# Kernel optimization log

Measured on AMD Instinct MI355X. Metric: run time of the kernel, lower is better.

The kernel has to match this reference:

```python
import jax, jax.numpy as jnp
import numpy as np

N_IN, N_HID, N_OUT = 2048, 4096, 1024
N_TOT = N_IN + N_HID + N_OUT
BATCH = 4096


def _structure_mask():
    # input -> {hidden, output}; hidden -> {hidden, output}; nothing feeds inputs,
    # outputs feed nothing.
    m = np.zeros((N_TOT, N_TOT), dtype=np.float32)
    m[0:N_IN, N_IN:N_TOT] = 1.0
    m[N_IN:N_IN + N_HID, N_IN:N_TOT] = 1.0
    return jnp.asarray(m)


def setup_inputs() -> dict:
    key = jax.random.key(0)
    kx, kw = jax.random.split(key)
    x = jax.random.normal(kx, (BATCH, N_IN), dtype=jnp.float32)
    weights = jax.random.normal(kw, (N_TOT, N_TOT), dtype=jnp.float32) * 0.1
    structure_mask = _structure_mask()
    return {"x": x, "weights": weights, "structure_mask": structure_mask}


def reference(x, weights, structure_mask):
    # Faithful to the torch forward: the per-neuron hidden loop reads the
    # activation vector BEFORE any hidden value is written, so every hidden
    # unit sees only [x, 0, 0]; outputs then see [x, hidden, 0].
    Wm = weights * structure_mask  # (N_TOT, N_TOT)
    B = x.shape[0]
    a0 = jnp.concatenate(
        [x, jnp.zeros((B, N_HID + N_OUT), dtype=x.dtype)], axis=1)  # (B, N_TOT)
    hidden = jax.nn.relu(a0 @ Wm[:, N_IN:N_IN + N_HID])             # (B, N_HID)
    a1 = jnp.concatenate(
        [x, hidden, jnp.zeros((B, N_OUT), dtype=x.dtype)], axis=1)  # (B, N_TOT)
    out = a1 @ Wm[:, N_IN + N_HID:]                                 # (B, N_OUT)
    return out
```

## Files before the change

kernel.cpp:

```cpp
#include <hip/hip_runtime.h>
#include <hip/hip_bf16.h>

#define N_IN  2048
#define N_HID 4096
#define N_OUT 1024
#define N_TOT 7168
#define BATCH 4096
#define LDA2  (N_IN + N_HID)
#define OUT_ELEMS ((size_t)BATCH * N_OUT)
#define BUF 16384

typedef __attribute__((ext_vector_type(8))) short short8;
typedef __attribute__((ext_vector_type(4))) float f32x4;

static __device__ __forceinline__ unsigned short f2bf(float f) {
  __hip_bfloat16 h = __float2bfloat16(f);
  return __builtin_bit_cast(unsigned short, h);
}

__global__ void conv_x_kernel(const float* __restrict__ x,
                              unsigned short* __restrict__ A2) {
  int idx = blockIdx.x * 256 + threadIdx.x;
  int row = idx >> 9;
  int col = (idx & 511) << 2;
  const float4 v = *(const float4*)(x + (size_t)row * N_IN + col);
  ushort4 o;
  o.x = f2bf(v.x); o.y = f2bf(v.y); o.z = f2bf(v.z); o.w = f2bf(v.w);
  *(ushort4*)(A2 + (size_t)row * LDA2 + col) = o;
}

__global__ void conv_t_kernel(const float* __restrict__ src, int lds_,
                              unsigned short* __restrict__ dst, int ldd) {
  __shared__ float tile[32][33];
  const int t = threadIdx.x;
  const int k0 = blockIdx.y << 5, n0 = blockIdx.x << 5;
  const int r = t >> 3, c = (t & 7) << 2;
  const float4 v = *(const float4*)(src + (size_t)(k0 + r) * lds_ + n0 + c);
  tile[r][c] = v.x; tile[r][c + 1] = v.y; tile[r][c + 2] = v.z; tile[r][c + 3] = v.w;
  __syncthreads();
  ushort4 o;
  o.x = f2bf(tile[c][r]);
  o.y = f2bf(tile[c + 1][r]);
  o.z = f2bf(tile[c + 2][r]);
  o.w = f2bf(tile[c + 3][r]);
  *(ushort4*)(dst + (size_t)(n0 + r) * ldd + k0 + c) = o;
}

__global__ void add5_kernel(const float* __restrict__ P, float* __restrict__ out) {
  size_t i = ((size_t)blockIdx.x * 256 + threadIdx.x) * 4;
  float4 a = *(const float4*)(P + i);
  float4 b = *(const float4*)(P + OUT_ELEMS + i);
  float4 c = *(const float4*)(P + 2 * OUT_ELEMS + i);
  float4 d = *(const float4*)(P + 3 * OUT_ELEMS + i);
  float4 e = *(const float4*)(P + 4 * OUT_ELEMS + i);
  float4 o;
  o.x = ((a.x + b.x) + (c.x + d.x)) + e.x;
  o.y = ((a.y + b.y) + (c.y + d.y)) + e.y;
  o.z = ((a.z + b.z) + (c.z + d.z)) + e.z;
  o.w = ((a.w + b.w) + (c.w + d.w)) + e.w;
  *(float4*)(out + i) = o;
}

struct KCtx {
  int wave, wm, wn, lm, quad, xr, srow, arow, brow;
};

static __device__ __forceinline__ void kctx_init(KCtx& c, int tid) {
  c.wave = tid >> 6;
  c.wm   = c.wave >> 2;
  c.wn   = c.wave & 3;
  c.lm   = tid & 15;
  c.quad = (tid & 63) >> 4;
  c.xr   = c.lm & 7;
  c.srow = c.wave * 16;
  c.arow = (c.wm * 128 + c.lm) * 64;
  c.brow = (c.wn * 64  + c.lm) * 64;
}

#define GLDS(GP, LP) __builtin_amdgcn_global_load_lds( \
    (const __attribute__((address_space(1))) void*)(GP), \
    (__attribute__((address_space(3))) void*)(LP), 16, 0, 0)

#define STG(GBASE, LD, LBASE, H, KC) do {                                     \
    GLDS((GBASE) + (size_t)((H)*128 + c.srow    ) * (LD) + (KC),              \
         (LBASE) + ((H)*128 + c.srow    ) * 64);                              \
    GLDS((GBASE) + (size_t)((H)*128 + c.srow + 8) * (LD) + (KC),              \
         (LBASE) + ((H)*128 + c.srow + 8) * 64);                              \
  } while (0)

#define LDB(BB) do {                                                          \
    _Pragma("unroll") for (int nt = 0; nt < 4; ++nt)                          \
    _Pragma("unroll") for (int kk = 0; kk < 2; ++kk)                          \
      bv[nt][kk] = *(const short8*)((BB) + c.brow + nt * 1024 +               \
                                    (((kk * 4 + c.quad) ^ c.xr) << 3));       \
  } while (0)

#define LDA_(AB, Q) do {                                                      \
    _Pragma("unroll") for (int j = 0; j < 2; ++j)                             \
    _Pragma("unroll") for (int kk = 0; kk < 2; ++kk)                          \
      av[j][kk] = *(const short8*)((AB) + c.arow + (2 * (Q) + j) * 1024 +     \
                                   (((kk * 4 + c.quad) ^ c.xr) << 3));        \
  } while (0)

#define MM(Q) do {                                                            \
    _Pragma("unroll") for (int kk = 0; kk < 2; ++kk)                          \
    _Pragma("unroll") for (int j = 0; j < 2; ++j)                             \
    _Pragma("unroll") for (int nt = 0; nt < 4; ++nt)                          \
      acc[2 * (Q) + j][nt] = __builtin_amdgcn_mfma_f32_16x16x32_bf16(         \
          av[j][kk], bv[nt][kk], acc[2 * (Q) + j][nt], 0, 0, 0);              \
  } while (0)

#define BAR       __builtin_amdgcn_s_barrier()
#define WAITLGKM  asm volatile("s_waitcnt lgkmcnt(0)" ::: "memory")
#define WAITVM4   asm volatile("s_waitcnt vmcnt(4)" ::: "memory")
#define WAITVM0   asm volatile("s_waitcnt vmcnt(0)" ::: "memory")
#define PRIO1     __builtin_amdgcn_s_setprio(1)
#define PRIO0     __builtin_amdgcn_s_setprio(0)

static __device__ __forceinline__ void kloop_256(
    const unsigned short* __restrict__ Agl,
    const unsigned short* __restrict__ Bgl,
    const int lda, const int ldb, const int kiters,
    unsigned short* __restrict__ S, const KCtx& c, f32x4 acc[8][4]) {
  unsigned short* const A0 = S;
  unsigned short* const A1 = S + BUF;
  unsigned short* const B0 = S + 2 * BUF;
  unsigned short* const B1 = S + 3 * BUF;

  short8 bv[4][2], av[2][2];

  STG(Agl, lda, A0, 0, 0); STG(Agl, lda, A0, 1, 0);
  STG(Bgl, ldb, B0, 0, 0); STG(Bgl, ldb, B0, 1, 0);
  STG(Bgl, ldb, B1, 0, 64); STG(Bgl, ldb, B1, 1, 64);
  WAITVM4;
  BAR;

#pragma unroll 1
  for (int i = 0; i < kiters - 1; ++i) {
    const int k1 = i * 128 + 64, k2 = i * 128 + 128, k3 = i * 128 + 192;
    LDB(B0); LDA_(A0, 0); STG(Agl, lda, A1, 0, k1);
    BAR; WAITLGKM; PRIO1; MM(0); PRIO0; BAR;
    LDA_(A0, 1); STG(Agl, lda, A1, 1, k1);
    BAR; WAITLGKM; PRIO1; MM(1); PRIO0; BAR;
    LDA_(A0, 2); STG(Bgl, ldb, B0, 0, k2);
    BAR; WAITLGKM; PRIO1; MM(2); PRIO0; BAR;
    LDA_(A0, 3); STG(Bgl, ldb, B0, 1, k2);
    WAITVM4; BAR; WAITLGKM; PRIO1; MM(3); PRIO0; BAR;
    LDB(B1); LDA_(A1, 0); STG(Agl, lda, A0, 0, k2);
    BAR; WAITLGKM; PRIO1; MM(0); PRIO0; BAR;
    LDA_(A1, 1); STG(Agl, lda, A0, 1, k2);
    BAR; WAITLGKM; PRIO1; MM(1); PRIO0; BAR;
    LDA_(A1, 2); STG(Bgl, ldb, B1, 0, k3);
    BAR; WAITLGKM; PRIO1; MM(2); PRIO0; BAR;
    LDA_(A1, 3); STG(Bgl, ldb, B1, 1, k3);
    WAITVM4; BAR; WAITLGKM; PRIO1; MM(3); PRIO0; BAR;
  }
  {
    const int k1 = (kiters - 1) * 128 + 64;
    LDB(B0); LDA_(A0, 0); STG(Agl, lda, A1, 0, k1);
    BAR; WAITLGKM; PRIO1; MM(0); PRIO0; BAR;
    LDA_(A0, 1); STG(Agl, lda, A1, 1, k1);
    BAR; WAITLGKM; PRIO1; MM(1); PRIO0; BAR;
    LDA_(A0, 2);
    BAR; WAITLGKM; PRIO1; MM(2); PRIO0; BAR;
    LDA_(A0, 3);
    WAITVM0; BAR; WAITLGKM; PRIO1; MM(3); PRIO0; BAR;
    LDB(B1); LDA_(A1, 0);
    BAR; WAITLGKM; PRIO1; MM(0); PRIO0; BAR;
    LDA_(A1, 1);
    BAR; WAITLGKM; PRIO1; MM(1); PRIO0; BAR;
    LDA_(A1, 2);
    BAR; WAITLGKM; PRIO1; MM(2); PRIO0; BAR;
    LDA_(A1, 3);
    BAR; WAITLGKM; PRIO1; MM(3); PRIO0; BAR;
  }
}

template <bool TO_BF16_RELU>
static __device__ __forceinline__ void epi_store(
    unsigned short* __restrict__ S, const KCtx& c, int tid, f32x4 acc[8][4],
    void* __restrict__ Cout, int ldc, int rowb, int colb) {
  float* Cf = (float*)S;
#pragma unroll 1
  for (int p = 0; p < 4; ++p) {
    if (c.wm == (p >> 1)) {
      const int mtb = (p & 1) * 4;
#pragma unroll
      for (int mt = 0; mt < 4; ++mt)
#pragma unroll
        for (int nt = 0; nt < 4; ++nt)
#pragma unroll
          for (int r = 0; r < 4; ++r)
            Cf[(mt * 16 + c.quad * 4 + r) * 260 + c.wn * 64 + nt * 16 + c.lm] =
                acc[mtb + mt][nt][r];
    }
    __syncthreads();
    const int c4 = (tid & 63) * 4;
    const int r0 = tid >> 6;
#pragma unroll
    for (int j = 0; j < 8; ++j) {
      const int row = r0 + 8 * j;
      float4 v = *(const float4*)(Cf + row * 260 + c4);
      if (TO_BF16_RELU) {
        ushort4 o;
        o.x = f2bf(v.x > 0.f ? v.x : 0.f);
        o.y = f2bf(v.y > 0.f ? v.y : 0.f);
        o.z = f2bf(v.z > 0.f ? v.z : 0.f);
        o.w = f2bf(v.w > 0.f ? v.w : 0.f);
        *(ushort4*)((unsigned short*)Cout +
                    (size_t)(rowb + p * 64 + row) * ldc + colb + c4) = o;
      } else {
        *(float4*)((float*)Cout +
                   (size_t)(rowb + p * 64 + row) * ldc + colb + c4) = v;
      }
    }
    __syncthreads();
  }
}

__global__ __launch_bounds__(512, 2)
void gemm_fused2(const unsigned short* __restrict__ A,
                 const unsigned short* __restrict__ Bt,
                 unsigned short* __restrict__ Hout,
                 float* __restrict__ P0) {
  __shared__ __align__(16) unsigned short S[4 * BUF];
  const int tid = threadIdx.x;
  const int lane = tid & 63;
  KCtx c; kctx_init(c, tid);
  const int bm = blockIdx.y, bn = blockIdx.x;
  const int gcol = ((lane & 7) ^ (lane >> 3)) << 3;

  const unsigned short* Agl = A  + (size_t)(bm * 256 + (lane >> 3)) * LDA2 + gcol;
  const unsigned short* Bgl = Bt + (size_t)(bn * 256 + (lane >> 3)) * N_IN + gcol;

  f32x4 acc[8][4];
#pragma unroll
  for (int i = 0; i < 8; ++i)
#pragma unroll
    for (int j = 0; j < 4; ++j)
      acc[i][j] = (f32x4){0.f, 0.f, 0.f, 0.f};

  kloop_256(Agl, Bgl, LDA2, N_IN, N_IN / 128, S, c, acc);
  __syncthreads();

  if (bn < 16)
    epi_store<true >(S, c, tid, acc, Hout, LDA2, bm * 256, bn * 256);
  else
    epi_store<false>(S, c, tid, acc, P0, N_OUT, bm * 256, (bn - 16) * 256);
}

__global__ __launch_bounds__(512, 2)
void gemm_p2(const unsigned short* __restrict__ A,
             const unsigned short* __restrict__ Bt,
             float* __restrict__ P) {
  __shared__ __align__(16) unsigned short S[4 * BUF];
  const int tid = threadIdx.x;
  const int lane = tid & 63;
  KCtx c; kctx_init(c, tid);
  const int bm = blockIdx.y, bn = blockIdx.x;
  const int ko0 = blockIdx.z * 1024;
  const int gcol = ((lane & 7) ^ (lane >> 3)) << 3;

  const unsigned short* Agl = A  + (size_t)(bm * 256 + (lane >> 3)) * LDA2 + gcol + ko0;
  const unsigned short* Bgl = Bt + (size_t)(bn * 256 + (lane >> 3)) * N_HID + gcol + ko0;

  f32x4 acc[8][4];
#pragma unroll
  for (int i = 0; i < 8; ++i)
#pragma unroll
    for (int j = 0; j < 4; ++j)
      acc[i][j] = (f32x4){0.f, 0.f, 0.f, 0.f};

  kloop_256(Agl, Bgl, LDA2, N_HID, 1024 / 128, S, c, acc);
  __syncthreads();

  epi_store<false>(S, c, tid, acc, P + (size_t)blockIdx.z * OUT_ELEMS, N_OUT,
                   bm * 256, bn * 256);
}

extern "C" void kernel_launch(void* const* d_in, const int* in_sizes, int n_in,
                              void* d_out, int out_size, void* d_ws, size_t ws_size,
                              hipStream_t stream) {
  const float* x = (const float*)d_in[0];
  const float* W = (const float*)d_in[1];

  char* ws = (char*)d_ws;
  const size_t A2_BYTES   = (size_t)BATCH * LDA2 * 2;
  const size_t BT12_BYTES = (size_t)(N_HID + N_OUT) * N_IN * 2;
  const size_t BT3_BYTES  = (size_t)N_OUT * N_HID * 2;
  unsigned short* A2   = (unsigned short*)ws;
  unsigned short* Bt12 = (unsigned short*)(ws + A2_BYTES);
  unsigned short* Bt3  = (unsigned short*)(ws + A2_BYTES + BT12_BYTES);
  float*          P    = (float*)(ws + A2_BYTES + BT12_BYTES + BT3_BYTES);

  conv_x_kernel<<<(BATCH * N_IN / 4) / 256, 256, 0, stream>>>(x, A2);

  conv_t_kernel<<<dim3((N_HID + N_OUT) / 32, N_IN / 32), 256, 0, stream>>>(
      W + N_IN, N_TOT, Bt12, N_IN);

  conv_t_kernel<<<dim3(N_OUT / 32, N_HID / 32), 256, 0, stream>>>(
      W + (size_t)N_IN * N_TOT + N_IN + N_HID, N_TOT, Bt3, N_HID);

  gemm_fused2<<<dim3((N_HID + N_OUT) / 256, BATCH / 256), 512, 0, stream>>>(
      A2, Bt12, A2 + N_IN, P);

  gemm_p2<<<dim3(N_OUT / 256, BATCH / 256, 4), 512, 0, stream>>>(
      A2 + N_IN, Bt3, P + OUT_ELEMS);

  add5_kernel<<<(OUT_ELEMS / 4) / 256, 256, 0, stream>>>(P, (float*)d_out);
}
```

Measured before the change: 571.3 us.

## Move output x-contribution into split-K second GEMM and drop LDS wait

The first GEMM now computes only the hidden layer, and the output GEMM runs over the concatenated [x, hidden] K dimension of 6144, split four ways into 1536-wide chunks. This removes a fifth partial buffer from the final reduction and balances the work between the two GEMMs. The main loop also drops the explicit lgkmcnt(0) waits, issues global-to-LDS loads before the LDS reads, and splits LDS into separate named arrays. The epilogue now goes through 16-row slices instead of 64-row slices, which adds barriers. Without the explicit waits, correctness depends on the compiler inserting the needed LDS waits itself.

```diff
diff --git a/kernel.cpp b/kernel.cpp
--- a/kernel.cpp
+++ b/kernel.cpp
@@ -46,18 +46,17 @@
   *(ushort4*)(dst + (size_t)(n0 + r) * ldd + k0 + c) = o;
 }
 
-__global__ void add5_kernel(const float* __restrict__ P, float* __restrict__ out) {
+__global__ void add4_kernel(const float* __restrict__ P, float* __restrict__ out) {
   size_t i = ((size_t)blockIdx.x * 256 + threadIdx.x) * 4;
   float4 a = *(const float4*)(P + i);
   float4 b = *(const float4*)(P + OUT_ELEMS + i);
   float4 c = *(const float4*)(P + 2 * OUT_ELEMS + i);
   float4 d = *(const float4*)(P + 3 * OUT_ELEMS + i);
-  float4 e = *(const float4*)(P + 4 * OUT_ELEMS + i);
   float4 o;
-  o.x = ((a.x + b.x) + (c.x + d.x)) + e.x;
-  o.y = ((a.y + b.y) + (c.y + d.y)) + e.y;
-  o.z = ((a.z + b.z) + (c.z + d.z)) + e.z;
-  o.w = ((a.w + b.w) + (c.w + d.w)) + e.w;
+  o.x = (a.x + b.x) + (c.x + d.x);
+  o.y = (a.y + b.y) + (c.y + d.y);
+  o.z = (a.z + b.z) + (c.z + d.z);
+  o.w = (a.w + b.w) + (c.w + d.w);
   *(float4*)(out + i) = o;
 }
 
@@ -81,11 +80,17 @@
     (const __attribute__((address_space(1))) void*)(GP), \
     (__attribute__((address_space(3))) void*)(LP), 16, 0, 0)
 
-#define STG(GBASE, LD, LBASE, H, KC) do {                                     \
-    GLDS((GBASE) + (size_t)((H)*128 + c.srow    ) * (LD) + (KC),              \
-         (LBASE) + ((H)*128 + c.srow    ) * 64);                              \
-    GLDS((GBASE) + (size_t)((H)*128 + c.srow + 8) * (LD) + (KC),              \
-         (LBASE) + ((H)*128 + c.srow + 8) * 64);                              \
+#define STGA(ARR, H, KC) do {                                                 \
+    GLDS(Agl + (size_t)((H)*128 + c.srow    ) * lda + (KC),                   \
+         (ARR) + ((H)*128 + c.srow    ) * 64);                                \
+    GLDS(Agl + (size_t)((H)*128 + c.srow + 8) * lda + (KC),                   \
+         (ARR) + ((H)*128 + c.srow + 8) * 64);                                \
+  } while (0)
+#define STGB(ARR, H, KC) do {                                                 \
+    GLDS(Bgl + (size_t)((H)*128 + c.srow    ) * ldb + (KC),                   \
+         (ARR) + ((H)*128 + c.srow    ) * 64);                                \
+    GLDS(Bgl + (size_t)((H)*128 + c.srow + 8) * ldb + (KC),                   \
+         (ARR) + ((H)*128 + c.srow + 8) * 64);                                \
   } while (0)
 
 #define LDB(BB) do {                                                          \
@@ -111,107 +116,103 @@
   } while (0)
 
 #define BAR       __builtin_amdgcn_s_barrier()
-#define WAITLGKM  asm volatile("s_waitcnt lgkmcnt(0)" ::: "memory")
 #define WAITVM4   asm volatile("s_waitcnt vmcnt(4)" ::: "memory")
 #define WAITVM0   asm volatile("s_waitcnt vmcnt(0)" ::: "memory")
 #define PRIO1     __builtin_amdgcn_s_setprio(1)
 #define PRIO0     __builtin_amdgcn_s_setprio(0)
 
 static __device__ __forceinline__ void kloop_256(
-    const unsigned short* __restrict__ Agl,
-    const unsigned short* __restrict__ Bgl,
+    const unsigned short* Agl, const unsigned short* Bgl,
     const int lda, const int ldb, const int kiters,
-    unsigned short* __restrict__ S, const KCtx& c, f32x4 acc[8][4]) {
-  unsigned short* const A0 = S;
-  unsigned short* const A1 = S + BUF;
-  unsigned short* const B0 = S + 2 * BUF;
-  unsigned short* const B1 = S + 3 * BUF;
-
+    unsigned short* A0s, unsigned short* A1s,
+    unsigned short* B0s, unsigned short* B1s,
+    const KCtx& c, f32x4 acc[8][4]) {
   short8 bv[4][2], av[2][2];
 
-  STG(Agl, lda, A0, 0, 0); STG(Agl, lda, A0, 1, 0);
-  STG(Bgl, ldb, B0, 0, 0); STG(Bgl, ldb, B0, 1, 0);
-  STG(Bgl, ldb, B1, 0, 64); STG(Bgl, ldb, B1, 1, 64);
+  STGA(A0s, 0, 0); STGA(A0s, 1, 0);
+  STGB(B0s, 0, 0); STGB(B0s, 1, 0);
+  STGB(B1s, 0, 64); STGB(B1s, 1, 64);
   WAITVM4;
   BAR;
 
 #pragma unroll 1
   for (int i = 0; i < kiters - 1; ++i) {
     const int k1 = i * 128 + 64, k2 = i * 128 + 128, k3 = i * 128 + 192;
-    LDB(B0); LDA_(A0, 0); STG(Agl, lda, A1, 0, k1);
-    BAR; WAITLGKM; PRIO1; MM(0); PRIO0; BAR;
-    LDA_(A0, 1); STG(Agl, lda, A1, 1, k1);
-    BAR; WAITLGKM; PRIO1; MM(1); PRIO0; BAR;
-    LDA_(A0, 2); STG(Bgl, ldb, B0, 0, k2);
-    BAR; WAITLGKM; PRIO1; MM(2); PRIO0; BAR;
-    LDA_(A0, 3); STG(Bgl, ldb, B0, 1, k2);
-    WAITVM4; BAR; WAITLGKM; PRIO1; MM(3); PRIO0; BAR;
-    LDB(B1); LDA_(A1, 0); STG(Agl, lda, A0, 0, k2);
-    BAR; WAITLGKM; PRIO1; MM(0); PRIO0; BAR;
-    LDA_(A1, 1); STG(Agl, lda, A0, 1, k2);
-    BAR; WAITLGKM; PRIO1; MM(1); PRIO0; BAR;
-    LDA_(A1, 2); STG(Bgl, ldb, B1, 0, k3);
-    BAR; WAITLGKM; PRIO1; MM(2); PRIO0; BAR;
-    LDA_(A1, 3); STG(Bgl, ldb, B1, 1, k3);
-    WAITVM4; BAR; WAITLGKM; PRIO1; MM(3); PRIO0; BAR;
+    STGA(A1s, 0, k1); LDB(B0s); LDA_(A0s, 0);
+    BAR; PRIO1; MM(0); PRIO0; BAR;
+    STGA(A1s, 1, k1); LDA_(A0s, 1);
+    BAR; PRIO1; MM(1); PRIO0; BAR;
+    STGB(B0s, 0, k2); LDA_(A0s, 2);
+    BAR; PRIO1; MM(2); PRIO0; BAR;
+    STGB(B0s, 1, k2); LDA_(A0s, 3);
+    WAITVM4;
+    BAR; PRIO1; MM(3); PRIO0; BAR;
+    STGA(A0s, 0, k2); LDB(B1s); LDA_(A1s, 0);
+    BAR; PRIO1; MM(0); PRIO0; BAR;
+    STGA(A0s, 1, k2); LDA_(A1s, 1);
+    BAR; PRIO1; MM(1); PRIO0; BAR;
+    STGB(B1s, 0, k3); LDA_(A1s, 2);
+    BAR; PRIO1; MM(2); PRIO0; BAR;
+    STGB(B1s, 1, k3); LDA_(A1s, 3);
+    WAITVM4;
+    BAR; PRIO1; MM(3); PRIO0; BAR;
   }
   {
-    const int k1 = (kiters - 1) * 128 + 64;
-    LDB(B0); LDA_(A0, 0); STG(Agl, lda, A1, 0, k1);
-    BAR; WAITLGKM; PRIO1; MM(0); PRIO0; BAR;
-    LDA_(A0, 1); STG(Agl, lda, A1, 1, k1);
-    BAR; WAITLGKM; PRIO1; MM(1); PRIO0; BAR;
-    LDA_(A0, 2);
-    BAR; WAITLGKM; PRIO1; MM(2); PRIO0; BAR;
-    LDA_(A0, 3);
-    WAITVM0; BAR; WAITLGKM; PRIO1; MM(3); PRIO0; BAR;
-    LDB(B1); LDA_(A1, 0);
-    BAR; WAITLGKM; PRIO1; MM(0); PRIO0; BAR;
-    LDA_(A1, 1);
-    BAR; WAITLGKM; PRIO1; MM(1); PRIO0; BAR;
-    LDA_(A1, 2);
-    BAR; WAITLGKM; PRIO1; MM(2); PRIO0; BAR;
-    LDA_(A1, 3);
-    BAR; WAITLGKM; PRIO1; MM(3); PRIO0; BAR;
+    const int kl = (kiters - 1) * 128 + 64;
+    STGA(A1s, 0, kl); LDB(B0s); LDA_(A0s, 0);
+    BAR; PRIO1; MM(0); PRIO0; BAR;
+    STGA(A1s, 1, kl); LDA_(A0s, 1);
+    BAR; PRIO1; MM(1); PRIO0; BAR;
+    LDA_(A0s, 2);
+    BAR; PRIO1; MM(2); PRIO0; BAR;
+    LDA_(A0s, 3);
+    WAITVM0;
+    BAR; PRIO1; MM(3); PRIO0; BAR;
+    LDB(B1s); LDA_(A1s, 0);
+    BAR; PRIO1; MM(0); PRIO0; BAR;
+    LDA_(A1s, 1);
+    BAR; PRIO1; MM(1); PRIO0; BAR;
+    LDA_(A1s, 2);
+    BAR; PRIO1; MM(2); PRIO0; BAR;
+    LDA_(A1s, 3);
+    BAR; PRIO1; MM(3); PRIO0; BAR;
   }
 }
 
-template <bool TO_BF16_RELU>
-static __device__ __forceinline__ void epi_store(
-    unsigned short* __restrict__ S, const KCtx& c, int tid, f32x4 acc[8][4],
-    void* __restrict__ Cout, int ldc, int rowb, int colb) {
-  float* Cf = (float*)S;
+template <bool RELU_BF16>
+static __device__ __forceinline__ void epi16(
+    unsigned short* B0s, const KCtx& c, int tid, f32x4 acc[8][4],
+    void* Cout, int ldc, int rowb, int colb) {
+  float* Epi = (float*)B0s;
+  const int row = tid >> 6;
+  const int col = (tid & 63) * 4;
 #pragma unroll 1
-  for (int p = 0; p < 4; ++p) {
-    if (c.wm == (p >> 1)) {
-      const int mtb = (p & 1) * 4;
-#pragma unroll
-      for (int mt = 0; mt < 4; ++mt)
-#pragma unroll
-        for (int nt = 0; nt < 4; ++nt)
-#pragma unroll
-          for (int r = 0; r < 4; ++r)
-            Cf[(mt * 16 + c.quad * 4 + r) * 260 + c.wn * 64 + nt * 16 + c.lm] =
-                acc[mtb + mt][nt][r];
+  for (int p = 0; p < 16; ++p) {
+    if (c.wm == (p >> 3)) {
+      const int mt = p & 7;
+#pragma unroll
+      for (int nt = 0; nt < 4; ++nt)
+#pragma unroll
+        for (int r = 0; r < 4; ++r)
+          Epi[(c.quad * 4 + r) * 260 + c.wn * 64 + nt * 16 + c.lm] =
+              acc[mt][nt][r];
     }
     __syncthreads();
-    const int c4 = (tid & 63) * 4;
-    const int r0 = tid >> 6;
-#pragma unroll
-    for (int j = 0; j < 8; ++j) {
-      const int row = r0 + 8 * j;
-      float4 v = *(const float4*)(Cf + row * 260 + c4);
-      if (TO_BF16_RELU) {
+#pragma unroll
+    for (int j = 0; j < 2; ++j) {
+      const int r2 = row + 8 * j;
+      float4 v = *(const float4*)(Epi + r2 * 260 + col);
+      if (RELU_BF16) {
         ushort4 o;
         o.x = f2bf(v.x > 0.f ? v.x : 0.f);
         o.y = f2bf(v.y > 0.f ? v.y : 0.f);
         o.z = f2bf(v.z > 0.f ? v.z : 0.f);
         o.w = f2bf(v.w > 0.f ? v.w : 0.f);
         *(ushort4*)((unsigned short*)Cout +
-                    (size_t)(rowb + p * 64 + row) * ldc + colb + c4) = o;
+                    (size_t)(rowb + p * 16 + r2) * ldc + colb + col) = o;
       } else {
         *(float4*)((float*)Cout +
-                   (size_t)(rowb + p * 64 + row) * ldc + colb + c4) = v;
+                   (size_t)(rowb + p * 16 + r2) * ldc + colb + col) = v;
       }
     }
     __syncthreads();
@@ -219,19 +220,22 @@
 }
 
 __global__ __launch_bounds__(512, 2)
-void gemm_fused2(const unsigned short* __restrict__ A,
-                 const unsigned short* __restrict__ Bt,
-                 unsigned short* __restrict__ Hout,
-                 float* __restrict__ P0) {
-  __shared__ __align__(16) unsigned short S[4 * BUF];
+void gemm1(const unsigned short* __restrict__ A,
+           const unsigned short* __restrict__ Bt,
+           unsigned short* __restrict__ Hout) {
+  __shared__ __align__(16) unsigned short A0s[BUF];
+  __shared__ __align__(16) unsigned short A1s[BUF];
+  __shared__ __align__(16) unsigned short B0s[BUF];
+  __shared__ __align__(16) unsigned short B1s[BUF];
   const int tid = threadIdx.x;
   const int lane = tid & 63;
   KCtx c; kctx_init(c, tid);
   const int bm = blockIdx.y, bn = blockIdx.x;
+  const int lda = LDA2, ldb = N_IN;
   const int gcol = ((lane & 7) ^ (lane >> 3)) << 3;
 
-  const unsigned short* Agl = A  + (size_t)(bm * 256 + (lane >> 3)) * LDA2 + gcol;
-  const unsigned short* Bgl = Bt + (size_t)(bn * 256 + (lane >> 3)) * N_IN + gcol;
+  const unsigned short* Agl = A  + (size_t)(bm * 256 + (lane >> 3)) * lda + gcol;
+  const unsigned short* Bgl = Bt + (size_t)(bn * 256 + (lane >> 3)) * ldb + gcol;
 
   f32x4 acc[8][4];
 #pragma unroll
@@ -240,29 +244,29 @@
     for (int j = 0; j < 4; ++j)
       acc[i][j] = (f32x4){0.f, 0.f, 0.f, 0.f};
 
-  kloop_256(Agl, Bgl, LDA2, N_IN, N_IN / 128, S, c, acc);
+  kloop_256(Agl, Bgl, lda, ldb, N_IN / 128, A0s, A1s, B0s, B1s, c, acc);
   __syncthreads();
-
-  if (bn < 16)
-    epi_store<true >(S, c, tid, acc, Hout, LDA2, bm * 256, bn * 256);
-  else
-    epi_store<false>(S, c, tid, acc, P0, N_OUT, bm * 256, (bn - 16) * 256);
+  epi16<true>(B0s, c, tid, acc, Hout, LDA2, bm * 256, bn * 256);
 }
 
 __global__ __launch_bounds__(512, 2)
-void gemm_p2(const unsigned short* __restrict__ A,
-             const unsigned short* __restrict__ Bt,
-             float* __restrict__ P) {
-  __shared__ __align__(16) unsigned short S[4 * BUF];
+void gemm2(const unsigned short* __restrict__ A,
+           const unsigned short* __restrict__ Bt,
+           float* __restrict__ P) {
+  __shared__ __align__(16) unsigned short A0s[BUF];
+  __shared__ __align__(16) unsigned short A1s[BUF];
+  __shared__ __align__(16) unsigned short B0s[BUF];
+  __shared__ __align__(16) unsigned short B1s[BUF];
   const int tid = threadIdx.x;
   const int lane = tid & 63;
   KCtx c; kctx_init(c, tid);
   const int bm = blockIdx.y, bn = blockIdx.x;
-  const int ko0 = blockIdx.z * 1024;
+  const int ko0 = blockIdx.z * 1536;
+  const int lda = LDA2, ldb = LDA2;
   const int gcol = ((lane & 7) ^ (lane >> 3)) << 3;
 
-  const unsigned short* Agl = A  + (size_t)(bm * 256 + (lane >> 3)) * LDA2 + gcol + ko0;
-  const unsigned short* Bgl = Bt + (size_t)(bn * 256 + (lane >> 3)) * N_HID + gcol + ko0;
+  const unsigned short* Agl = A  + (size_t)(bm * 256 + (lane >> 3)) * lda + gcol + ko0;
+  const unsigned short* Bgl = Bt + (size_t)(bn * 256 + (lane >> 3)) * ldb + gcol + ko0;
 
   f32x4 acc[8][4];
 #pragma unroll
@@ -271,11 +275,10 @@
     for (int j = 0; j < 4; ++j)
       acc[i][j] = (f32x4){0.f, 0.f, 0.f, 0.f};
 
-  kloop_256(Agl, Bgl, LDA2, N_HID, 1024 / 128, S, c, acc);
+  kloop_256(Agl, Bgl, lda, ldb, 1536 / 128, A0s, A1s, B0s, B1s, c, acc);
   __syncthreads();
-
-  epi_store<false>(S, c, tid, acc, P + (size_t)blockIdx.z * OUT_ELEMS, N_OUT,
-                   bm * 256, bn * 256);
+  epi16<false>(B0s, c, tid, acc, P + (size_t)blockIdx.z * OUT_ELEMS, N_OUT,
+               bm * 256, bn * 256);
 }
 
 extern "C" void kernel_launch(void* const* d_in, const int* in_sizes, int n_in,
@@ -286,26 +289,26 @@
 
   char* ws = (char*)d_ws;
   const size_t A2_BYTES   = (size_t)BATCH * LDA2 * 2;
-  const size_t BT12_BYTES = (size_t)(N_HID + N_OUT) * N_IN * 2;
-  const size_t BT3_BYTES  = (size_t)N_OUT * N_HID * 2;
+  const size_t BT1_BYTES  = (size_t)N_HID * N_IN * 2;
+  const size_t BT23_BYTES = (size_t)N_OUT * LDA2 * 2;
   unsigned short* A2   = (unsigned short*)ws;
-  unsigned short* Bt12 = (unsigned short*)(ws + A2_BYTES);
-  unsigned short* Bt3  = (unsigned short*)(ws + A2_BYTES + BT12_BYTES);
-  float*          P    = (float*)(ws + A2_BYTES + BT12_BYTES + BT3_BYTES);
+  unsigned short* Bt1  = (unsigned short*)(ws + A2_BYTES);
+  unsigned short* Bt23 = (unsigned short*)(ws + A2_BYTES + BT1_BYTES);
+  float*          P    = (float*)(ws + A2_BYTES + BT1_BYTES + BT23_BYTES);
 
   conv_x_kernel<<<(BATCH * N_IN / 4) / 256, 256, 0, stream>>>(x, A2);
 
-  conv_t_kernel<<<dim3((N_HID + N_OUT) / 32, N_IN / 32), 256, 0, stream>>>(
-      W + N_IN, N_TOT, Bt12, N_IN);
-
-  conv_t_kernel<<<dim3(N_OUT / 32, N_HID / 32), 256, 0, stream>>>(
-      W + (size_t)N_IN * N_TOT + N_IN + N_HID, N_TOT, Bt3, N_HID);
-
-  gemm_fused2<<<dim3((N_HID + N_OUT) / 256, BATCH / 256), 512, 0, stream>>>(
-      A2, Bt12, A2 + N_IN, P);
-
-  gemm_p2<<<dim3(N_OUT / 256, BATCH / 256, 4), 512, 0, stream>>>(
-      A2 + N_IN, Bt3, P + OUT_ELEMS);
-
-  add5_kernel<<<(OUT_ELEMS / 4) / 256, 256, 0, stream>>>(P, (float*)d_out);
-}
+  conv_t_kernel<<<dim3(N_HID / 32, N_IN / 32), 256, 0, stream>>>(
+      W + N_IN, N_TOT, Bt1, N_IN);
+
+  conv_t_kernel<<<dim3(N_OUT / 32, LDA2 / 32), 256, 0, stream>>>(
+      W + N_IN + N_HID, N_TOT, Bt23, LDA2);
+
+  gemm1<<<dim3(N_HID / 256, BATCH / 256), 512, 0, stream>>>(
+      A2, Bt1, A2 + N_IN);
+
+  gemm2<<<dim3(N_OUT / 256, BATCH / 256, 4), 512, 0, stream>>>(
+      A2, Bt23, P);
+
+  add4_kernel<<<(OUT_ELEMS / 4) / 256, 256, 0, stream>>>(P, (float*)d_out);
+}
```

New measurement: 537.9 us. -5.9%, faster.
